# Kernel tuning notes

Hardware: AMD Instinct MI355X
Metric: run time of the kernel (lower is better)

## Reference

```python
import jax, jax.numpy as jnp
import numpy as np

B, N, D, H = 2, 1024, 768, 16
HD = D // H          # head_dim = 48
HID = 2 * D          # transition hidden = 1536
EPS = 1e-5


def _ln(x, w=None, b=None):
    m = x.mean(-1, keepdims=True)
    v = ((x - m) ** 2).mean(-1, keepdims=True)
    y = (x - m) * jax.lax.rsqrt(v + EPS)
    if w is not None:
        y = y * w
    if b is not None:
        y = y + b
    return y


def _adaln(a, s, snw, ssw, ssb, sbw):
    # a: LN without affine; s: LN with weight only; sigmoid-gated scale + bias
    an = _ln(a)
    sn = _ln(s, snw)
    return an * jax.nn.sigmoid(sn @ ssw + ssb) + sn @ sbw


def setup_inputs() -> dict:
    key = jax.random.key(0)
    ks = jax.random.split(key, 20)
    w = 0.02

    def nrm(k, shape, scale=1.0):
        return jax.random.normal(k, shape, jnp.float32) * scale

    return {
        "a": nrm(ks[0], (B, N, D)),
        "s": nrm(ks[1], (B, N, D)),
        "z": nrm(ks[2], (H, B, N, N), 0.1),  # pair bias, fed as attn mask
        "adaln1_snw": jnp.ones((D,), jnp.float32),
        "adaln1_ssw": nrm(ks[3], (D, D), w),
        "adaln1_ssb": jnp.zeros((D,), jnp.float32),
        "adaln1_sbw": nrm(ks[4], (D, D), w),
        "q_w": nrm(ks[5], (D, D), w),
        "q_b": jnp.zeros((D,), jnp.float32),
        "k_w": nrm(ks[6], (D, D), w),
        "v_w": nrm(ks[7], (D, D), w),
        "g_w": nrm(ks[8], (D, D), w),
        "o_w": nrm(ks[9], (D, D), w),
        "outproj_w": nrm(ks[10], (D, D), w),
        "outproj_b": jnp.zeros((D,), jnp.float32),
        "adaln2_snw": jnp.ones((D,), jnp.float32),
        "adaln2_ssw": nrm(ks[11], (D, D), w),
        "adaln2_ssb": jnp.zeros((D,), jnp.float32),
        "adaln2_sbw": nrm(ks[12], (D, D), w),
        "swish_w": nrm(ks[13], (D, 2 * HID), w),
        "a2b_w": nrm(ks[14], (D, HID), w),
        "b2a_w": nrm(ks[15], (HID, D), w),
        "op_w": nrm(ks[16], (D, D), w),
        "op_b": jnp.zeros((D,), jnp.float32),
    }


def reference(a, s, z,
              adaln1_snw, adaln1_ssw, adaln1_ssb, adaln1_sbw,
              q_w, q_b, k_w, v_w, g_w, o_w,
              outproj_w, outproj_b,
              adaln2_snw, adaln2_ssw, adaln2_ssb, adaln2_sbw,
              swish_w, a2b_w, b2a_w, op_w, op_b):
    # --- AdaLN then pair-bias attention ---
    b = _adaln(a, s, adaln1_snw, adaln1_ssw, adaln1_ssb, adaln1_sbw)

    q = (b @ q_w + q_b).reshape(B, N, H, HD)  # head split: outer H, inner HD
    k = (b @ k_w).reshape(B, N, H, HD)
    v = (b @ v_w).reshape(B, N, H, HD)

    scores = jnp.einsum('bqhd,bkhd->hbqk', q, k) * (HD ** -0.5) + z
    p = jax.nn.softmax(scores, axis=-1)
    o = jnp.einsum('hbqk,bkhd->bqhd', p, v).reshape(B, N, D)

    g = jax.nn.sigmoid(b @ g_w)
    x = (o * g) @ o_w

    # sigmoid-gated residual (AdaLN-zero-style output projection on s)
    a = a + jax.nn.sigmoid(s @ outproj_w + outproj_b) * x

    # --- ConditionedTransitionBlock ---
    a2 = _adaln(a, s, adaln2_snw, adaln2_ssw, adaln2_ssb, adaln2_sbw)
    sw = a2 @ swish_w                     # [B, N, 2*HID]
    u, gate = sw[..., :HID], sw[..., HID:]
    hidden = jax.nn.silu(gate) * u * (a2 @ a2b_w)
    t = jax.nn.sigmoid(s @ op_w + op_b) * (hidden @ b2a_w)

    return a + t
```

## Files before the change

### kernel.cpp

```cpp
#include <hip/hip_runtime.h>
#include <math.h>

constexpr int CB = 2, CN = 1024, CD = 768, CH = 16, CHD = 48, CHID = 1536;
constexpr int CT = CB * CN;
constexpr float CEPS = 1e-5f;

typedef __bf16 bf16_t;
typedef __bf16 bf16x8 __attribute__((ext_vector_type(8)));
typedef __bf16 bf16x4 __attribute__((ext_vector_type(4)));
typedef float  f32x4  __attribute__((ext_vector_type(4)));

__device__ __forceinline__ float sigf(float x) { return 1.f / (1.f + expf(-x)); }

__device__ __forceinline__ void gload16(const void* g, void* l) {
    __builtin_amdgcn_global_load_lds((const __attribute__((address_space(1))) void*)g,
                                     (__attribute__((address_space(3))) void*)l, 16, 0, 0);
}

__global__ __launch_bounds__(256) void ln_pre_k(
    const float* __restrict__ a, const float* __restrict__ s,
    const float* __restrict__ snw,
    float* __restrict__ an, bf16_t* __restrict__ snbf, bf16_t* __restrict__ sbf)
{
    __shared__ float r4[4][4];
    const int row = blockIdx.x;
    const int tid = threadIdx.x;
    const float* ar = a + (size_t)row * CD;
    const float* sr = s + (size_t)row * CD;

    float av[3], sv[3];
    float suma = 0.f, sqa = 0.f, sums = 0.f, sqs = 0.f;
#pragma unroll
    for (int j = 0; j < 3; ++j) {
        const int i = tid + j * 256;
        av[j] = ar[i]; sv[j] = sr[i];
        suma += av[j]; sqa += av[j] * av[j];
        sums += sv[j]; sqs += sv[j] * sv[j];
    }
#pragma unroll
    for (int o = 32; o > 0; o >>= 1) {
        suma += __shfl_down(suma, o, 64);
        sqa  += __shfl_down(sqa,  o, 64);
        sums += __shfl_down(sums, o, 64);
        sqs  += __shfl_down(sqs,  o, 64);
    }
    const int wv = tid >> 6;
    if ((tid & 63) == 0) { r4[0][wv] = suma; r4[1][wv] = sqa; r4[2][wv] = sums; r4[3][wv] = sqs; }
    __syncthreads();
    suma = r4[0][0] + r4[0][1] + r4[0][2] + r4[0][3];
    sqa  = r4[1][0] + r4[1][1] + r4[1][2] + r4[1][3];
    sums = r4[2][0] + r4[2][1] + r4[2][2] + r4[2][3];
    sqs  = r4[3][0] + r4[3][1] + r4[3][2] + r4[3][3];

    const float inv_d = 1.f / (float)CD;
    const float ma = suma * inv_d;
    const float ra = rsqrtf(sqa * inv_d - ma * ma + CEPS);
    const float ms = sums * inv_d;
    const float rs = rsqrtf(sqs * inv_d - ms * ms + CEPS);

#pragma unroll
    for (int j = 0; j < 3; ++j) {
        const int i = tid + j * 256;
        an[(size_t)row * CD + i]   = (av[j] - ma) * ra;
        snbf[(size_t)row * CD + i] = (bf16_t)((sv[j] - ms) * rs * snw[i]);
        if (sbf) sbf[(size_t)row * CD + i] = (bf16_t)sv[j];
    }
}

__global__ __launch_bounds__(256) void tcvt_k(
    const float* __restrict__ src, const int ld_src, const int col_ofs,
    bf16_t* __restrict__ dst, const int ld_dst, const int row_ofs)
{
    __shared__ float t[32][33];
    const int k0 = blockIdx.y * 32, n0 = blockIdx.x * 32;
    const int tx = threadIdx.x & 31, ty = threadIdx.x >> 5;
#pragma unroll
    for (int i = 0; i < 4; ++i)
        t[ty + 8 * i][tx] = src[(size_t)(k0 + ty + 8 * i) * ld_src + col_ofs + n0 + tx];
    __syncthreads();
#pragma unroll
    for (int i = 0; i < 4; ++i)
        dst[(size_t)(row_ofs + n0 + ty + 8 * i) * ld_dst + k0 + tx] = (bf16_t)t[tx][ty + 8 * i];
}

template<bool CBF16>
__global__ __launch_bounds__(256) void mgemm_k(
    const bf16_t* __restrict__ A, const int lda,
    const bf16_t* __restrict__ Bt, const int K,
    void* __restrict__ Cv, const int ldc)
{
    __shared__ __align__(16) bf16_t lA[2][128 * 32];
    __shared__ __align__(16) bf16_t lB[2][128 * 32];
    const int tid  = threadIdx.x;
    const int lane = tid & 63;
    const int m0 = blockIdx.y * 128;
    const int n0 = blockIdx.x * 128;
    const int wv = tid >> 6;
    const int wr = (wv >> 1) * 64;
    const int wc = (wv & 1) * 64;

    f32x4 acc[4][4] = {};

    const int r0 = tid >> 2,        kg0 = (tid & 3) * 8;
    const int r1 = (tid + 256) >> 2, kg1 = kg0;
    const int wbase = (tid & ~63) * 16;

#define STAGE(buf, kt)                                                                  \
    do {                                                                                \
        gload16(A  + (size_t)(m0 + r0) * lda + (kt) + kg0, (char*)lA[buf] + wbase);     \
        gload16(A  + (size_t)(m0 + r1) * lda + (kt) + kg1, (char*)lA[buf] + 4096 + wbase); \
        gload16(Bt + (size_t)(n0 + r0) * K   + (kt) + kg0, (char*)lB[buf] + wbase);     \
        gload16(Bt + (size_t)(n0 + r1) * K   + (kt) + kg1, (char*)lB[buf] + 4096 + wbase); \
    } while (0)

    const int nt = K >> 5;
    STAGE(0, 0);
    __syncthreads();

    const int afr = wr + (lane & 15);
    const int bfr_ = wc + (lane & 15);
    const int kof = (lane >> 4) * 8;

    for (int t = 0; t < nt; ++t) {
        const int buf = t & 1;
        if (t + 1 < nt) STAGE(buf ^ 1, (t + 1) << 5);
        bf16x8 af[4], bfv[4];
#pragma unroll
        for (int i = 0; i < 4; ++i) {
            af[i]  = *(const bf16x8*)&lA[buf][(afr + i * 16) * 32 + kof];
            bfv[i] = *(const bf16x8*)&lB[buf][(bfr_ + i * 16) * 32 + kof];
        }
#pragma unroll
        for (int mi = 0; mi < 4; ++mi)
#pragma unroll
            for (int ni = 0; ni < 4; ++ni)
                acc[mi][ni] = __builtin_amdgcn_mfma_f32_16x16x32_bf16(af[mi], bfv[ni], acc[mi][ni], 0, 0, 0);
        __syncthreads();
    }
#undef STAGE

    const int crow = m0 + wr + ((lane >> 4) << 2);
    const int ccol = n0 + wc + (lane & 15);
#pragma unroll
    for (int mi = 0; mi < 4; ++mi)
#pragma unroll
        for (int r = 0; r < 4; ++r) {
            const size_t ro = (size_t)(crow + mi * 16 + r) * ldc + ccol;
#pragma unroll
            for (int ni = 0; ni < 4; ++ni) {
                if (CBF16) ((bf16_t*)Cv)[ro + ni * 16] = (bf16_t)acc[mi][ni][r];
                else       ((float*)Cv)[ro + ni * 16]  = acc[mi][ni][r];
            }
        }
}

__global__ __launch_bounds__(256) void comb_adaln_k(
    const float* __restrict__ an, const bf16_t* __restrict__ ssb_mat,
    const float* __restrict__ bias, bf16_t* __restrict__ out)
{
    const int i4 = (blockIdx.x * 256 + threadIdx.x) * 4;
    const int row = i4 / CD, col = i4 - row * CD;
    const float4 anv = *(const float4*)&an[i4];
    const bf16x4 ssv = *(const bf16x4*)&ssb_mat[(size_t)row * 1536 + col];
    const bf16x4 sbv = *(const bf16x4*)&ssb_mat[(size_t)row * 1536 + 768 + col];
    const float4 bv  = *(const float4*)&bias[col];
    bf16x4 o;
    o[0] = (bf16_t)(anv.x * sigf((float)ssv[0] + bv.x) + (float)sbv[0]);
    o[1] = (bf16_t)(anv.y * sigf((float)ssv[1] + bv.y) + (float)sbv[1]);
    o[2] = (bf16_t)(anv.z * sigf((float)ssv[2] + bv.z) + (float)sbv[2]);
    o[3] = (bf16_t)(anv.w * sigf((float)ssv[3] + bv.w) + (float)sbv[3]);
    *(bf16x4*)&out[i4] = o;
}

__global__ __launch_bounds__(256) void gateadd_k(
    const float* __restrict__ base, const float* __restrict__ gates, const int g_ofs,
    const float* __restrict__ bias, const float* __restrict__ x, float* __restrict__ dst)
{
    const int i4 = (blockIdx.x * 256 + threadIdx.x) * 4;
    const int row = i4 / CD, col = i4 - row * CD;
    const float4 bv = *(const float4*)&base[i4];
    const float4 gv = *(const float4*)&gates[(size_t)row * 1536 + g_ofs + col];
    const float4 bi = *(const float4*)&bias[col];
    const float4 xv = *(const float4*)&x[i4];
    float4 o;
    o.x = bv.x + sigf(gv.x + bi.x) * xv.x;
    o.y = bv.y + sigf(gv.y + bi.y) * xv.y;
    o.z = bv.z + sigf(gv.z + bi.z) * xv.z;
    o.w = bv.w + sigf(gv.w + bi.w) * xv.w;
    *(float4*)&dst[i4] = o;
}

__global__ __launch_bounds__(256) void mlp_comb_k(
    const bf16_t* __restrict__ ugh, bf16_t* __restrict__ hidden)
{
    const int i4 = (blockIdx.x * 256 + threadIdx.x) * 4;
    const int row = i4 / CHID, col = i4 - row * CHID;
    const bf16x4 uv = *(const bf16x4*)&ugh[(size_t)row * 4608 + col];
    const bf16x4 gv = *(const bf16x4*)&ugh[(size_t)row * 4608 + 1536 + col];
    const bf16x4 hv = *(const bf16x4*)&ugh[(size_t)row * 4608 + 3072 + col];
    bf16x4 o;
#pragma unroll
    for (int j = 0; j < 4; ++j) {
        const float g = (float)gv[j];
        o[j] = (bf16_t)(g * sigf(g) * (float)uv[j] * (float)hv[j]);
    }
    *(bf16x4*)&hidden[i4] = o;
}

__global__ __launch_bounds__(256) void attn_k(
    const float* __restrict__ qkvg, const float* __restrict__ qb,
    const float* __restrict__ z, bf16_t* __restrict__ og)
{
    __shared__ float kls[64][52];
    __shared__ float vls[64][52];
    const int tid  = threadIdx.x;
    const int qb_i = blockIdx.x;
    const int h    = blockIdx.y;
    const int b    = blockIdx.z;
    const int r    = tid >> 2;
    const int quad = tid & 3;
    const int qrow = qb_i * 64 + r;
    const float scale = 0.14433756729740643f;

    float qreg[48];
    const float* qp = qkvg + (size_t)(b * CN + qrow) * 3072 + h * CHD;
#pragma unroll
    for (int j = 0; j < 12; ++j) {
        const float4 t4 = *(const float4*)(qp + j * 4);
        const float4 b4 = *(const float4*)(qb + h * CHD + j * 4);
        qreg[j * 4 + 0] = t4.x + b4.x; qreg[j * 4 + 1] = t4.y + b4.y;
        qreg[j * 4 + 2] = t4.z + b4.z; qreg[j * 4 + 3] = t4.w + b4.w;
    }
    float acc[48];
#pragma unroll
    for (int d = 0; d < 48; ++d) acc[d] = 0.f;
    float m = -1e30f, l = 0.f;

    const float* zbase = z + (((size_t)(h * CB + b)) * CN + qrow) * CN;
    const float* kbase = qkvg + 768  + h * CHD;
    const float* vbase = qkvg + 1536 + h * CHD;

    for (int kt = 0; kt < CN; kt += 64) {
        __syncthreads();
#pragma unroll
        for (int j = 0; j < 3; ++j) {
            const int idx = tid + j * 256;
            const int key = idx / 12;
            const int d4  = idx - key * 12;
            const size_t gofs = (size_t)(b * CN + kt + key) * 3072 + d4 * 4;
            *(float4*)&kls[key][d4 * 4] = *(const float4*)(kbase + gofs);
            *(float4*)&vls[key][d4 * 4] = *(const float4*)(vbase + gofs);
        }
        __syncthreads();

        float sc[16];
#pragma unroll
        for (int kk = 0; kk < 16; ++kk) {
            const int key = kk * 4 + quad;
            float dt = 0.f;
#pragma unroll
            for (int j = 0; j < 12; ++j) {
                const float4 k4 = *(const float4*)&kls[key][j * 4];
                dt = fmaf(qreg[j * 4 + 0], k4.x, dt);
                dt = fmaf(qreg[j * 4 + 1], k4.y, dt);
                dt = fmaf(qreg[j * 4 + 2], k4.z, dt);
                dt = fmaf(qreg[j * 4 + 3], k4.w, dt);
            }
            sc[kk] = dt * scale + zbase[kt + key];
        }
        float tmax = sc[0];
#pragma unroll
        for (int kk = 1; kk < 16; ++kk) tmax = fmaxf(tmax, sc[kk]);
        tmax = fmaxf(tmax, __shfl_xor(tmax, 1, 4));
        tmax = fmaxf(tmax, __shfl_xor(tmax, 2, 4));
        const float mnew = fmaxf(m, tmax);
        const float resc = expf(m - mnew);
        m = mnew;
        l *= resc;
#pragma unroll
        for (int d = 0; d < 48; ++d) acc[d] *= resc;

        float p[16]; float ps = 0.f;
#pragma unroll
        for (int kk = 0; kk < 16; ++kk) { p[kk] = expf(sc[kk] - mnew); ps += p[kk]; }
        l += ps;

#pragma unroll
        for (int kk = 0; kk < 16; ++kk) {
            const int key = kk * 4 + quad;
            const float pv = p[kk];
#pragma unroll
            for (int j = 0; j < 12; ++j) {
                const float4 v4 = *(const float4*)&vls[key][j * 4];
                acc[j * 4 + 0] = fmaf(pv, v4.x, acc[j * 4 + 0]);
                acc[j * 4 + 1] = fmaf(pv, v4.y, acc[j * 4 + 1]);
                acc[j * 4 + 2] = fmaf(pv, v4.z, acc[j * 4 + 2]);
                acc[j * 4 + 3] = fmaf(pv, v4.w, acc[j * 4 + 3]);
            }
        }
    }

    l += __shfl_xor(l, 1, 4);
    l += __shfl_xor(l, 2, 4);
    const float inv = 1.f / l;
#pragma unroll
    for (int d = 0; d < 48; ++d) {
        acc[d] += __shfl_xor(acc[d], 1, 4);
        acc[d] += __shfl_xor(acc[d], 2, 4);
    }
    if (quad == 0) {
        const float* gp = qkvg + (size_t)(b * CN + qrow) * 3072 + 2304 + h * CHD;
        bf16_t* op = og + (size_t)(b * CN + qrow) * CD + h * CHD;
#pragma unroll
        for (int j = 0; j < 12; ++j) {
            const float4 gv = *(const float4*)(gp + j * 4);
            bf16x4 o;
            o[0] = (bf16_t)(acc[j * 4 + 0] * inv * sigf(gv.x));
            o[1] = (bf16_t)(acc[j * 4 + 1] * inv * sigf(gv.y));
            o[2] = (bf16_t)(acc[j * 4 + 2] * inv * sigf(gv.z));
            o[3] = (bf16_t)(acc[j * 4 + 3] * inv * sigf(gv.w));
            *(bf16x4*)(op + j * 4) = o;
        }
    }
}

extern "C" void kernel_launch(void* const* d_in, const int* in_sizes, int n_in,
                              void* d_out, int out_size, void* d_ws, size_t ws_size,
                              hipStream_t stream)
{
    const float* a       = (const float*)d_in[0];
    const float* s       = (const float*)d_in[1];
    const float* z       = (const float*)d_in[2];
    const float* a1_snw  = (const float*)d_in[3];
    const float* a1_ssw  = (const float*)d_in[4];
    const float* a1_ssb  = (const float*)d_in[5];
    const float* a1_sbw  = (const float*)d_in[6];
    const float* q_w     = (const float*)d_in[7];
    const float* q_b     = (const float*)d_in[8];
    const float* k_w     = (const float*)d_in[9];
    const float* v_w     = (const float*)d_in[10];
    const float* g_w     = (const float*)d_in[11];
    const float* o_w     = (const float*)d_in[12];
    const float* outproj_w = (const float*)d_in[13];
    const float* outproj_b = (const float*)d_in[14];
    const float* a2_snw  = (const float*)d_in[15];
    const float* a2_ssw  = (const float*)d_in[16];
    const float* a2_ssb  = (const float*)d_in[17];
    const float* a2_sbw  = (const float*)d_in[18];
    const float* swish_w = (const float*)d_in[19];
    const float* a2b_w   = (const float*)d_in[20];
    const float* b2a_w   = (const float*)d_in[21];
    const float* op_w    = (const float*)d_in[22];
    const float* op_b    = (const float*)d_in[23];
    float* out = (float*)d_out;
    char*  wsb = (char*)d_ws;

    size_t off = 0;
    auto alloc = [&](size_t bytes) { char* p = wsb + off; off = (off + bytes + 255) & ~(size_t)255; return p; };
    float*  A_an    = (float*) alloc((size_t)CT * CD * 4);
    bf16_t* B_sn    = (bf16_t*)alloc((size_t)CT * CD * 2);
    bf16_t* C_sbf   = (bf16_t*)alloc((size_t)CT * CD * 2);
    bf16_t* D_ssb   = (bf16_t*)alloc((size_t)CT * 1536 * 2);
    bf16_t* E_act   = (bf16_t*)alloc((size_t)CT * CD * 2);
    char*   F_big   = (char*)  alloc((size_t)CT * 3072 * 4);
    float*  G_gates = (float*) alloc((size_t)CT * 1536 * 4);
    float*  H_anew  = (float*) alloc((size_t)CT * CD * 4);
    float*  J_x     = (float*) alloc((size_t)CT * CD * 4);
    bf16_t* W1t     = (bf16_t*)alloc((size_t)1536 * 768 * 2);
    bf16_t* W2t     = (bf16_t*)alloc((size_t)1536 * 768 * 2);
    bf16_t* Wqkvgt  = (bf16_t*)alloc((size_t)3072 * 768 * 2);
    bf16_t* Wgt     = (bf16_t*)alloc((size_t)1536 * 768 * 2);
    bf16_t* W3t     = (bf16_t*)alloc((size_t)4608 * 768 * 2);
    bf16_t* Wot     = (bf16_t*)alloc((size_t)768 * 768 * 2);
    bf16_t* Wb2at   = (bf16_t*)alloc((size_t)768 * 1536 * 2);
    float*  qkvg_f  = (float*)F_big;
    bf16_t* ugh_b   = (bf16_t*)F_big;
    bf16_t* hidden  = D_ssb;
    float*  y2      = A_an;

    const dim3 blk(256);
    const dim3 t88(24, 24);
    tcvt_k<<<t88, blk, 0, stream>>>(a1_ssw, 768, 0, W1t, 768, 0);
    tcvt_k<<<t88, blk, 0, stream>>>(a1_sbw, 768, 0, W1t, 768, 768);
    tcvt_k<<<t88, blk, 0, stream>>>(q_w, 768, 0, Wqkvgt, 768, 0);
    tcvt_k<<<t88, blk, 0, stream>>>(k_w, 768, 0, Wqkvgt, 768, 768);
    tcvt_k<<<t88, blk, 0, stream>>>(v_w, 768, 0, Wqkvgt, 768, 1536);
    tcvt_k<<<t88, blk, 0, stream>>>(g_w, 768, 0, Wqkvgt, 768, 2304);
    tcvt_k<<<t88, blk, 0, stream>>>(outproj_w, 768, 0, Wgt, 768, 0);
    tcvt_k<<<t88, blk, 0, stream>>>(op_w, 768, 0, Wgt, 768, 768);
    tcvt_k<<<t88, blk, 0, stream>>>(a2_ssw, 768, 0, W2t, 768, 0);
    tcvt_k<<<t88, blk, 0, stream>>>(a2_sbw, 768, 0, W2t, 768, 768);
    tcvt_k<<<dim3(48, 24), blk, 0, stream>>>(swish_w, 3072, 0,    W3t, 768, 0);
    tcvt_k<<<dim3(48, 24), blk, 0, stream>>>(swish_w, 3072, 1536, W3t, 768, 1536);
    tcvt_k<<<dim3(48, 24), blk, 0, stream>>>(a2b_w, 1536, 0,      W3t, 768, 3072);
    tcvt_k<<<t88, blk, 0, stream>>>(o_w, 768, 0, Wot, 768, 0);
    tcvt_k<<<dim3(24, 48), blk, 0, stream>>>(b2a_w, 768, 0, Wb2at, 1536, 0);

    const dim3 e768(CT * CD / 4 / 256);
    const dim3 e1536(CT * CHID / 4 / 256);
#define GRID(N) dim3((N) / 128, CT / 128)

    ln_pre_k<<<CT, blk, 0, stream>>>(a, s, a1_snw, A_an, B_sn, C_sbf);
    mgemm_k<true ><<<GRID(1536), blk, 0, stream>>>(B_sn, CD, W1t, 768, D_ssb, 1536);
    comb_adaln_k<<<e768, blk, 0, stream>>>(A_an, D_ssb, a1_ssb, E_act);
    mgemm_k<false><<<GRID(3072), blk, 0, stream>>>(E_act, CD, Wqkvgt, 768, qkvg_f, 3072);
    mgemm_k<false><<<GRID(1536), blk, 0, stream>>>(C_sbf, CD, Wgt, 768, G_gates, 1536);
    attn_k<<<dim3(CN / 64, CH, CB), blk, 0, stream>>>(qkvg_f, q_b, z, E_act);
    mgemm_k<false><<<GRID(768), blk, 0, stream>>>(E_act, CD, Wot, 768, J_x, 768);
    gateadd_k<<<e768, blk, 0, stream>>>(a, G_gates, 0, outproj_b, J_x, H_anew);
    ln_pre_k<<<CT, blk, 0, stream>>>(H_anew, s, a2_snw, A_an, B_sn, nullptr);
    mgemm_k<true ><<<GRID(1536), blk, 0, stream>>>(B_sn, CD, W2t, 768, D_ssb, 1536);
    comb_adaln_k<<<e768, blk, 0, stream>>>(A_an, D_ssb, a2_ssb, E_act);
    mgemm_k<true ><<<GRID(4608), blk, 0, stream>>>(E_act, CD, W3t, 768, ugh_b, 4608);
    mlp_comb_k<<<e1536, blk, 0, stream>>>(ugh_b, hidden);
    mgemm_k<false><<<GRID(768), blk, 0, stream>>>(hidden, CHID, Wb2at, 1536, y2, 768);
    gateadd_k<<<e768, blk, 0, stream>>>(H_anew, G_gates, 768, op_b, y2, out);
#undef GRID

    (void)in_sizes; (void)n_in; (void)out_size; (void)ws_size;
}
```

Before: 590.8 us.

## Batch weight transposes into one launch and split attention keys across eight lanes

The fifteen weight transpose-convert launches are merged into one kernel that uses a job table to map each block to its source matrix. The attention kernel now gives each query row eight lanes instead of four and covers 32 queries per block, which doubles the grid size and halves the per-thread key work. The aim is to cut launch overhead and raise attention parallelism and occupancy, in exchange for an extra shuffle reduction stage and a K/V tile load into shared memory that is amortized over fewer queries.

Result: slower. 720.9 us (+22.0%).

```diff
diff --git a/kernel.cpp b/kernel.cpp
--- a/kernel.cpp
+++ b/kernel.cpp
@@ -67,12 +67,22 @@
     }
 }
 
-__global__ __launch_bounds__(256) void tcvt_k(
-    const float* __restrict__ src, const int ld_src, const int col_ofs,
-    bf16_t* __restrict__ dst, const int ld_dst, const int row_ofs)
+struct TJob { const float* src; bf16_t* dst; int ld_src, col_ofs, ld_dst, row_ofs, ntx, cnt; };
+struct TJobs { TJob j[15]; };
+
+__global__ __launch_bounds__(256) void tcvt_all_k(TJobs jobs)
 {
     __shared__ float t[32][33];
-    const int k0 = blockIdx.y * 32, n0 = blockIdx.x * 32;
+    int tb = blockIdx.x;
+    int ji = 0;
+    while (ji < 14 && tb >= jobs.j[ji].cnt) { tb -= jobs.j[ji].cnt; ++ji; }
+    const float* src = jobs.j[ji].src;
+    bf16_t* dst      = jobs.j[ji].dst;
+    const int ld_src = jobs.j[ji].ld_src, col_ofs = jobs.j[ji].col_ofs;
+    const int ld_dst = jobs.j[ji].ld_dst, row_ofs = jobs.j[ji].row_ofs;
+    const int ntx    = jobs.j[ji].ntx;
+    const int n0 = (tb % ntx) * 32;
+    const int k0 = (tb / ntx) * 32;
     const int tx = threadIdx.x & 31, ty = threadIdx.x >> 5;
 #pragma unroll
     for (int i = 0; i < 4; ++i)
@@ -217,9 +227,9 @@
     const int qb_i = blockIdx.x;
     const int h    = blockIdx.y;
     const int b    = blockIdx.z;
-    const int r    = tid >> 2;
-    const int quad = tid & 3;
-    const int qrow = qb_i * 64 + r;
+    const int r    = tid >> 3;
+    const int oct  = tid & 7;
+    const int qrow = qb_i * 32 + r;
     const float scale = 0.14433756729740643f;
 
     float qreg[48];
@@ -253,10 +263,10 @@
         }
         __syncthreads();
 
-        float sc[16];
-#pragma unroll
-        for (int kk = 0; kk < 16; ++kk) {
-            const int key = kk * 4 + quad;
+        float sc[8];
+#pragma unroll
+        for (int kk = 0; kk < 8; ++kk) {
+            const int key = kk * 8 + oct;
             float dt = 0.f;
 #pragma unroll
             for (int j = 0; j < 12; ++j) {
@@ -266,13 +276,14 @@
                 dt = fmaf(qreg[j * 4 + 2], k4.z, dt);
                 dt = fmaf(qreg[j * 4 + 3], k4.w, dt);
             }
-            sc[kk] = dt * scale + zbase[kt + key];
+            sc[kk] = dt * scale + zbase[kt + kk * 8 + oct];
         }
         float tmax = sc[0];
 #pragma unroll
-        for (int kk = 1; kk < 16; ++kk) tmax = fmaxf(tmax, sc[kk]);
-        tmax = fmaxf(tmax, __shfl_xor(tmax, 1, 4));
-        tmax = fmaxf(tmax, __shfl_xor(tmax, 2, 4));
+        for (int kk = 1; kk < 8; ++kk) tmax = fmaxf(tmax, sc[kk]);
+        tmax = fmaxf(tmax, __shfl_xor(tmax, 1, 8));
+        tmax = fmaxf(tmax, __shfl_xor(tmax, 2, 8));
+        tmax = fmaxf(tmax, __shfl_xor(tmax, 4, 8));
         const float mnew = fmaxf(m, tmax);
         const float resc = expf(m - mnew);
         m = mnew;
@@ -280,14 +291,14 @@
 #pragma unroll
         for (int d = 0; d < 48; ++d) acc[d] *= resc;
 
-        float p[16]; float ps = 0.f;
-#pragma unroll
-        for (int kk = 0; kk < 16; ++kk) { p[kk] = expf(sc[kk] - mnew); ps += p[kk]; }
+        float p[8]; float ps = 0.f;
+#pragma unroll
+        for (int kk = 0; kk < 8; ++kk) { p[kk] = expf(sc[kk] - mnew); ps += p[kk]; }
         l += ps;
 
 #pragma unroll
-        for (int kk = 0; kk < 16; ++kk) {
-            const int key = kk * 4 + quad;
+        for (int kk = 0; kk < 8; ++kk) {
+            const int key = kk * 8 + oct;
             const float pv = p[kk];
 #pragma unroll
             for (int j = 0; j < 12; ++j) {
@@ -300,15 +311,17 @@
         }
     }
 
-    l += __shfl_xor(l, 1, 4);
-    l += __shfl_xor(l, 2, 4);
+    l += __shfl_xor(l, 1, 8);
+    l += __shfl_xor(l, 2, 8);
+    l += __shfl_xor(l, 4, 8);
     const float inv = 1.f / l;
 #pragma unroll
     for (int d = 0; d < 48; ++d) {
-        acc[d] += __shfl_xor(acc[d], 1, 4);
-        acc[d] += __shfl_xor(acc[d], 2, 4);
-    }
-    if (quad == 0) {
+        acc[d] += __shfl_xor(acc[d], 1, 8);
+        acc[d] += __shfl_xor(acc[d], 2, 8);
+        acc[d] += __shfl_xor(acc[d], 4, 8);
+    }
+    if (oct == 0) {
         const float* gp = qkvg + (size_t)(b * CN + qrow) * 3072 + 2304 + h * CHD;
         bf16_t* op = og + (size_t)(b * CN + qrow) * CD + h * CHD;
 #pragma unroll
@@ -379,22 +392,25 @@
     float*  y2      = A_an;
 
     const dim3 blk(256);
-    const dim3 t88(24, 24);
-    tcvt_k<<<t88, blk, 0, stream>>>(a1_ssw, 768, 0, W1t, 768, 0);
-    tcvt_k<<<t88, blk, 0, stream>>>(a1_sbw, 768, 0, W1t, 768, 768);
-    tcvt_k<<<t88, blk, 0, stream>>>(q_w, 768, 0, Wqkvgt, 768, 0);
-    tcvt_k<<<t88, blk, 0, stream>>>(k_w, 768, 0, Wqkvgt, 768, 768);
-    tcvt_k<<<t88, blk, 0, stream>>>(v_w, 768, 0, Wqkvgt, 768, 1536);
-    tcvt_k<<<t88, blk, 0, stream>>>(g_w, 768, 0, Wqkvgt, 768, 2304);
-    tcvt_k<<<t88, blk, 0, stream>>>(outproj_w, 768, 0, Wgt, 768, 0);
-    tcvt_k<<<t88, blk, 0, stream>>>(op_w, 768, 0, Wgt, 768, 768);
-    tcvt_k<<<t88, blk, 0, stream>>>(a2_ssw, 768, 0, W2t, 768, 0);
-    tcvt_k<<<t88, blk, 0, stream>>>(a2_sbw, 768, 0, W2t, 768, 768);
-    tcvt_k<<<dim3(48, 24), blk, 0, stream>>>(swish_w, 3072, 0,    W3t, 768, 0);
-    tcvt_k<<<dim3(48, 24), blk, 0, stream>>>(swish_w, 3072, 1536, W3t, 768, 1536);
-    tcvt_k<<<dim3(48, 24), blk, 0, stream>>>(a2b_w, 1536, 0,      W3t, 768, 3072);
-    tcvt_k<<<t88, blk, 0, stream>>>(o_w, 768, 0, Wot, 768, 0);
-    tcvt_k<<<dim3(24, 48), blk, 0, stream>>>(b2a_w, 768, 0, Wb2at, 1536, 0);
+
+    TJobs tj = {{
+        {a1_ssw,    W1t,    768,  0,    768,  0,    24, 576},
+        {a1_sbw,    W1t,    768,  0,    768,  768,  24, 576},
+        {q_w,       Wqkvgt, 768,  0,    768,  0,    24, 576},
+        {k_w,       Wqkvgt, 768,  0,    768,  768,  24, 576},
+        {v_w,       Wqkvgt, 768,  0,    768,  1536, 24, 576},
+        {g_w,       Wqkvgt, 768,  0,    768,  2304, 24, 576},
+        {outproj_w, Wgt,    768,  0,    768,  0,    24, 576},
+        {op_w,      Wgt,    768,  0,    768,  768,  24, 576},
+        {a2_ssw,    W2t,    768,  0,    768,  0,    24, 576},
+        {a2_sbw,    W2t,    768,  0,    768,  768,  24, 576},
+        {swish_w,   W3t,    3072, 0,    768,  0,    48, 1152},
+        {swish_w,   W3t,    3072, 1536, 768,  1536, 48, 1152},
+        {a2b_w,     W3t,    1536, 0,    768,  3072, 48, 1152},
+        {o_w,       Wot,    768,  0,    768,  0,    24, 576},
+        {b2a_w,     Wb2at,  768,  0,    1536, 0,    24, 1152},
+    }};
+    tcvt_all_k<<<dim3(10944), blk, 0, stream>>>(tj);
 
     const dim3 e768(CT * CD / 4 / 256);
     const dim3 e1536(CT * CHID / 4 / 256);
@@ -405,7 +421,7 @@
     comb_adaln_k<<<e768, blk, 0, stream>>>(A_an, D_ssb, a1_ssb, E_act);
     mgemm_k<false><<<GRID(3072), blk, 0, stream>>>(E_act, CD, Wqkvgt, 768, qkvg_f, 3072);
     mgemm_k<false><<<GRID(1536), blk, 0, stream>>>(C_sbf, CD, Wgt, 768, G_gates, 1536);
-    attn_k<<<dim3(CN / 64, CH, CB), blk, 0, stream>>>(qkvg_f, q_b, z, E_act);
+    attn_k<<<dim3(CN / 32, CH, CB), blk, 0, stream>>>(qkvg_f, q_b, z, E_act);
     mgemm_k<false><<<GRID(768), blk, 0, stream>>>(E_act, CD, Wot, 768, J_x, 768);
     gateadd_k<<<e768, blk, 0, stream>>>(a, G_gates, 0, outproj_b, J_x, H_anew);
     ln_pre_k<<<CT, blk, 0, stream>>>(H_anew, s, a2_snw, A_an, B_sn, nullptr);
```
